# Kernel optimization log

Measured on AMD Instinct MI355X. Metric: run time of the kernel, lower is better.

The kernel has to match this reference:

```python
import jax, jax.numpy as jnp
import numpy as np

N = 8192   # number of points
K = 16     # knn_graph k (loop=True -> self included)
C = 256    # conv hidden width
H = 128    # classifier hidden width


def _lin_init(key, fan_in, fan_out):
    s = 1.0 / np.sqrt(fan_in)
    kw, kb = jax.random.split(key)
    W = jax.random.uniform(kw, (fan_in, fan_out), minval=-s, maxval=s, dtype=jnp.float32)
    b = jax.random.uniform(kb, (fan_out,), minval=-s, maxval=s, dtype=jnp.float32)
    return W, b


def setup_inputs() -> dict:
    key = jax.random.key(0)
    ks = jax.random.split(key, 10)
    pos = jax.random.normal(ks[0], (N, 3), dtype=jnp.float32)
    # conv1 local_nn: Linear(3+3,256), ReLU, Linear(256,256)
    c1_W1, c1_b1 = _lin_init(ks[1], 3 + 3, C)
    c1_W2, c1_b2 = _lin_init(ks[2], C, C)
    # conv2/conv3 local_nn: Linear(256+3,256), ReLU, Linear(256,256)
    c2_W1, c2_b1 = _lin_init(ks[3], C + 3, C)
    c2_W2, c2_b2 = _lin_init(ks[4], C, C)
    c3_W1, c3_b1 = _lin_init(ks[5], C + 3, C)
    c3_W2, c3_b2 = _lin_init(ks[6], C, C)
    # classifier: Linear(256,128), ReLU, Linear(128,128), ReLU, Linear(128,1)
    h_W1, h_b1 = _lin_init(ks[7], C, H)
    h_W2, h_b2 = _lin_init(ks[8], H, H)
    h_W3, h_b3 = _lin_init(ks[9], H, 1)
    return dict(pos=pos,
                c1_W1=c1_W1, c1_b1=c1_b1, c1_W2=c1_W2, c1_b2=c1_b2,
                c2_W1=c2_W1, c2_b1=c2_b1, c2_W2=c2_W2, c2_b2=c2_b2,
                c3_W1=c3_W1, c3_b1=c3_b1, c3_W2=c3_W2, c3_b2=c3_b2,
                h_W1=h_W1, h_b1=h_b1, h_W2=h_W2, h_b2=h_b2, h_W3=h_W3, h_b3=h_b3)


def _knn_idx(pos):
    # squared pairwise distances via the gram trick; [N,N]
    sq = jnp.sum(pos * pos, axis=-1)
    d2 = sq[:, None] + sq[None, :] - 2.0 * (pos @ pos.T)
    # k smallest distances (self distance ~0 -> self loop, matching loop=True)
    _, idx = jax.lax.top_k(-d2, K)  # [N,K] neighbor (source) indices per target
    return idx


def _pointnet_conv(h, rel, idx, W1, b1, W2, b2):
    # message = local_nn(concat(x_j, pos_j - pos_i)); aggregate = max over neighbors
    e = jnp.concatenate([h[idx], rel], axis=-1)          # [N,K,Cin+3]
    m = jax.nn.relu(e @ W1 + b1) @ W2 + b2               # [N,K,C]
    return jnp.max(m, axis=1)                            # [N,C]


def reference(pos,
              c1_W1, c1_b1, c1_W2, c1_b2,
              c2_W1, c2_b1, c2_W2, c2_b2,
              c3_W1, c3_b1, c3_W2, c3_b2,
              h_W1, h_b1, h_W2, h_b2, h_W3, h_b3):
    idx = _knn_idx(pos)
    rel = pos[idx] - pos[:, None, :]                     # [N,K,3] relative coords
    h = pos                                              # train_with_norm=False
    h = jax.nn.relu(_pointnet_conv(h, rel, idx, c1_W1, c1_b1, c1_W2, c1_b2))
    h = jax.nn.relu(_pointnet_conv(h, rel, idx, c2_W1, c2_b1, c2_W2, c2_b2))
    h = jax.nn.relu(_pointnet_conv(h, rel, idx, c3_W1, c3_b1, c3_W2, c3_b2))
    h = jax.nn.relu(h @ h_W1 + h_b1)
    h = jax.nn.relu(h @ h_W2 + h_b2)
    return jax.nn.sigmoid(h @ h_W3 + h_b3)               # [N,1]
```

## Files before the change

### kernel.cpp

```cpp
#include <hip/hip_runtime.h>
#include <hip/hip_bf16.h>
#include <math.h>

#define NPTS 8192
#define CDIM 256
#define HDIM 128
#define NCH  32
#define CH   (NPTS / NCH)
#define CAP  48

typedef __attribute__((ext_vector_type(8))) short bf16x8;
typedef __attribute__((ext_vector_type(4))) float f32x4;
typedef unsigned long long u64;

static __device__ __forceinline__ short f2bf(float f) {
  __hip_bfloat16 h = __float2bfloat16(f);
  return *reinterpret_cast<short*>(&h);
}
static __device__ __forceinline__ float bf2f(short s) {
  return __uint_as_float(((unsigned)(unsigned short)s) << 16);
}

static __device__ __forceinline__ unsigned umed3(unsigned a, unsigned b,
                                                 unsigned c) {
  unsigned d;
  asm("v_med3_u32 %0, %1, %2, %3" : "=v"(d) : "v"(a), "v"(b), "v"(c));
  return d;
}

static __device__ __forceinline__ unsigned d2key(float4 p, float4 c) {
  float dot = fmaf(p.x, c.x, fmaf(p.y, c.y, p.z * c.z));
  float d2 = fmaf(-2.0f, dot, p.w + c.w);
  return __float_as_uint(fmaxf(d2, 0.0f));
}

#define U32INIT unsigned b0=~0u,b1=~0u,b2=~0u,b3=~0u,b4=~0u,b5=~0u,b6=~0u, \
                         b7=~0u,b8=~0u,b9=~0u,b10=~0u,b11=~0u,b12=~0u, \
                         b13=~0u,b14=~0u,b15=~0u;
#define U32CHAIN(key) { \
  b15 = umed3(b14, key, b15); b14 = umed3(b13, key, b14); \
  b13 = umed3(b12, key, b13); b12 = umed3(b11, key, b12); \
  b11 = umed3(b10, key, b11); b10 = umed3(b9,  key, b10); \
  b9  = umed3(b8,  key, b9);  b8  = umed3(b7,  key, b8);  \
  b7  = umed3(b6,  key, b7);  b6  = umed3(b5,  key, b6);  \
  b5  = umed3(b4,  key, b5);  b4  = umed3(b3,  key, b4);  \
  b3  = umed3(b2,  key, b3);  b2  = umed3(b1,  key, b2);  \
  b1  = umed3(b0,  key, b1);  b0  = min(b0, key); }

#define KSTEP(s) { bool sw_ = key < k##s; u64 t_ = k##s; \
                   k##s = sw_ ? key : t_; key = sw_ ? t_ : key; }
#define KCHAIN KSTEP(0) KSTEP(1) KSTEP(2) KSTEP(3) KSTEP(4) KSTEP(5) \
               KSTEP(6) KSTEP(7) KSTEP(8) KSTEP(9) KSTEP(10) KSTEP(11) \
               KSTEP(12) KSTEP(13) KSTEP(14) KSTEP(15)
#define KINIT u64 k0=~0ULL,k1=~0ULL,k2=~0ULL,k3=~0ULL,k4=~0ULL,k5=~0ULL, \
                  k6=~0ULL,k7=~0ULL,k8=~0ULL,k9=~0ULL,k10=~0ULL,k11=~0ULL, \
                  k12=~0ULL,k13=~0ULL,k14=~0ULL,k15=~0ULL;

__global__ __launch_bounds__(256) void prep_all(
    const float* __restrict__ c1W2, const float* __restrict__ c2W2,
    const float* __restrict__ c3W2, const float* __restrict__ c2W1,
    const float* __restrict__ c3W1, const float* __restrict__ hW1,
    const float* __restrict__ hW2,
    short* __restrict__ w2f1, short* __restrict__ w2f2,
    short* __restrict__ w2f3, short* __restrict__ wc2a,
    short* __restrict__ wc3a, short* __restrict__ whW1,
    short* __restrict__ whW2,
    const float* __restrict__ pos, float4* __restrict__ pos4,
    const float* __restrict__ c1W1, const float* __restrict__ c1b1,
    short* __restrict__ TU) {
  int b = blockIdx.x, tid = threadIdx.x;
  if (b < 1280) {
    const float* W; short* wf; int rb;
    if (b < 256)       { W = c1W2; wf = w2f1; rb = b; }
    else if (b < 512)  { W = c2W2; wf = w2f2; rb = b - 256; }
    else if (b < 768)  { W = c3W2; wf = w2f3; rb = b - 512; }
    else if (b < 1024) { W = c2W1; wf = wc2a; rb = b - 768; }
    else               { W = c3W1; wf = wc3a; rb = b - 1024; }
    int t = rb * 256 + tid;
    int q = t & 7, l = (t >> 3) & 63, F = t >> 9;
    int ks = F & 7, c16 = F >> 3;
    int k = ks * 32 + ((l >> 4) << 3) + q;
    int c = c16 * 16 + (l & 15);
    wf[t] = f2bf(W[k * 256 + c]);
  } else if (b < 1408) {
    int t = (b - 1280) * 256 + tid;
    int q = t & 7, l = (t >> 3) & 63, F = t >> 9;
    int ks = F & 7, c16 = F >> 3;
    int k = ks * 32 + ((l >> 4) << 3) + q;
    int c = c16 * 16 + (l & 15);
    whW1[t] = f2bf(hW1[k * 128 + c]);
  } else if (b < 1472) {
    int t = (b - 1408) * 256 + tid;
    int q = t & 7, l = (t >> 3) & 63, F = t >> 9;
    int ks = F & 3, c16 = F >> 2;
    int k = ks * 32 + ((l >> 4) << 3) + q;
    int c = c16 * 16 + (l & 15);
    whW2[t] = f2bf(hW2[k * 128 + c]);
  } else if (b < 1504) {
    int i = (b - 1472) * 256 + tid;
    float x = pos[3 * i], y = pos[3 * i + 1], z = pos[3 * i + 2];
    pos4[i] = make_float4(x, y, z, x * x + y * y + z * z);
  } else {
    int c = tid;
    float w0 = c1W1[c]       + c1W1[768 + c];
    float w1 = c1W1[256 + c] + c1W1[1024 + c];
    float w2 = c1W1[512 + c] + c1W1[1280 + c];
    float bv = c1b1[c];
    int i0 = (b - 1504) * 16;
#pragma unroll
    for (int r = 0; r < 16; ++r) {
      int i = i0 + r;
      float x = pos[3 * i], y = pos[3 * i + 1], z = pos[3 * i + 2];
      TU[(size_t)i * 256 + c] = f2bf(fmaf(x, w0, fmaf(y, w1, fmaf(z, w2, bv))));
    }
  }
}

__global__ __launch_bounds__(256) void knn_d2p1(const float4* __restrict__ pos4,
                                                unsigned* __restrict__ v) {
  int ch = blockIdx.x & (NCH - 1);
  int i  = (blockIdx.x >> 5) * 256 + threadIdx.x;
  const float4* cb = pos4 + ch * CH;

  float4 p = pos4[i];
  U32INIT
  for (int jj = 0; jj < CH; jj += 4) {
    float4 c0 = cb[jj], c1 = cb[jj + 1], c2 = cb[jj + 2], c3 = cb[jj + 3];
    unsigned x0 = d2key(p, c0), x1 = d2key(p, c1);
    unsigned x2 = d2key(p, c2), x3 = d2key(p, c3);
    U32CHAIN(x0) U32CHAIN(x1) U32CHAIN(x2) U32CHAIN(x3)
  }
  uint4* dst = reinterpret_cast<uint4*>(v + ((size_t)ch * NPTS + i) * 16);
  dst[0] = make_uint4(b0, b1, b2, b3);
  dst[1] = make_uint4(b4, b5, b6, b7);
  dst[2] = make_uint4(b8, b9, b10, b11);
  dst[3] = make_uint4(b12, b13, b14, b15);
}

__global__ __launch_bounds__(256) void knn_merge(const unsigned* __restrict__ v,
                                                 unsigned* __restrict__ T,
                                                 unsigned* __restrict__ cnt) {
  int wv = threadIdx.x >> 6, lane = threadIdx.x & 63;
  int i = blockIdx.x * 4 + wv;
  int ch = lane >> 1, half = lane & 1;
  const uint4* src = reinterpret_cast<const uint4*>(
      v + ((size_t)ch * NPTS + i) * 16 + half * 8);
  uint4 a = src[0], b = src[1];
  unsigned r1 = a.y, r2 = a.z, r3 = a.w;
  unsigned r4 = b.x, r5 = b.y, r6 = b.z, r7 = b.w;
  unsigned h = a.x;
  unsigned wmin = 0;
#pragma unroll
  for (int round = 0; round < 16; ++round) {
    unsigned m = h;
    m = min(m, (unsigned)__shfl_xor((int)m, 1));
    m = min(m, (unsigned)__shfl_xor((int)m, 2));
    m = min(m, (unsigned)__shfl_xor((int)m, 4));
    m = min(m, (unsigned)__shfl_xor((int)m, 8));
    m = min(m, (unsigned)__shfl_xor((int)m, 16));
    m = min(m, (unsigned)__shfl_xor((int)m, 32));
    wmin = m;
    u64 ball = __ballot(h == m);
    bool adv = (lane == __ffsll(ball) - 1);
    h  = adv ? r1 : h;
    r1 = adv ? r2 : r1;
    r2 = adv ? r3 : r2;
    r3 = adv ? r4 : r3;
    r4 = adv ? r5 : r4;
    r5 = adv ? r6 : r5;
    r6 = adv ? r7 : r6;
    r7 = adv ? 0xFFFFFFFFu : r7;
  }
  if (lane == 0) { T[i] = wmin; cnt[i] = 0; }
}

__global__ __launch_bounds__(256) void knn_d2p2(const float4* __restrict__ pos4,
                                                const unsigned* __restrict__ T,
                                                unsigned* __restrict__ cnt,
                                                u64* __restrict__ cbuf) {
  int ch = blockIdx.x & (NCH - 1);
  int i  = (blockIdx.x >> 5) * 256 + threadIdx.x;
  const float4* cb = pos4 + ch * CH;

  float4 p = pos4[i];
  unsigned Ti = T[i];
  int jb = ch * CH;
  for (int jj = 0; jj < CH; jj += 8) {
    unsigned k[8];
#pragma unroll
    for (int u = 0; u < 8; ++u) k[u] = d2key(p, cb[jj + u]);
    unsigned m = min(min(min(k[0], k[1]), min(k[2], k[3])),
                     min(min(k[4], k[5]), min(k[6], k[7])));
    if (m <= Ti) {
#pragma unroll
      for (int u = 0; u < 8; ++u) {
        if (k[u] <= Ti) {
          unsigned slot = atomicAdd(&cnt[i], 1u);
          if (slot < CAP)
            cbuf[(size_t)i * CAP + slot] =
                ((u64)k[u] << 32) | (unsigned)(jb + jj + u);
        }
      }
    }
  }
}

__global__ __launch_bounds__(256) void knn_select(const unsigned* __restrict__ cnt,
                                                  const u64* __restrict__ cbuf,
                                                  int* __restrict__ idx_out) {
  int i = blockIdx.x * 256 + threadIdx.x;
  int c = (int)min(cnt[i], (unsigned)CAP);
  KINIT
#pragma unroll 1
  for (int q = 0; q < c; ++q) {
    u64 key = cbuf[(size_t)i * CAP + q];
    if (key < k15) { KCHAIN }
  }
  int* o = idx_out + i * 16;
  o[0]=(int)(unsigned)k0;   o[1]=(int)(unsigned)k1;   o[2]=(int)(unsigned)k2;
  o[3]=(int)(unsigned)k3;   o[4]=(int)(unsigned)k4;   o[5]=(int)(unsigned)k5;
  o[6]=(int)(unsigned)k6;   o[7]=(int)(unsigned)k7;   o[8]=(int)(unsigned)k8;
  o[9]=(int)(unsigned)k9;   o[10]=(int)(unsigned)k10; o[11]=(int)(unsigned)k11;
  o[12]=(int)(unsigned)k12; o[13]=(int)(unsigned)k13; o[14]=(int)(unsigned)k14;
  o[15]=(int)(unsigned)k15;
}

template <int NCOLS, int KDIM, int ACT, int ADDP, int OUTBF>
__global__ __launch_bounds__(256) void gemm_mfma(
    const short* __restrict__ A,
    const short* __restrict__ wf,
    const float* __restrict__ bias,
    const float* __restrict__ pos,
    const float* __restrict__ W1p,
    void* __restrict__ outp) {
  constexpr int KS = KDIM / 32;
  constexpr int NF = NCOLS / 64;
  __shared__ __align__(16) short As[32 * KDIM];

  int tid = threadIdx.x;
  int row0 = blockIdx.x * 32;

  {
    int row = tid & 31, wq = tid >> 5;
    const short* Ar = A + (size_t)(row0 + row) * KDIM;
#pragma unroll
    for (int q = 0; q < KDIM / 64; ++q) {
      int c0 = wq * 8 + q * 64;
      bf16x8 o = *reinterpret_cast<const bf16x8*>(Ar + c0);
      int byte = row * (KDIM * 2) + c0 * 2;
      byte ^= (row & 7) << 4;
      *reinterpret_cast<bf16x8*>(reinterpret_cast<char*>(As) + byte) = o;
    }
  }
  __syncthreads();

  int l = tid & 63, w = tid >> 6;
  int lhi = l >> 4, llo = l & 15;
  f32x4 zero = {0.f, 0.f, 0.f, 0.f};
  f32x4 acc[2][NF];
#pragma unroll
  for (int m = 0; m < 2; ++m)
#pragma unroll
    for (int n = 0; n < NF; ++n) acc[m][n] = zero;

  const bf16x8* WfV = reinterpret_cast<const bf16x8*>(wf);
#pragma unroll
  for (int ks = 0; ks < KS; ++ks) {
    bf16x8 af[2], bfr[NF];
#pragma unroll
    for (int m = 0; m < 2; ++m) {
      int r = m * 16 + llo;
      int byte = r * (KDIM * 2) + ks * 64 + lhi * 16;
      byte ^= (r & 7) << 4;
      af[m] = *reinterpret_cast<const bf16x8*>(
          reinterpret_cast<const char*>(As) + byte);
    }
#pragma unroll
    for (int n = 0; n < NF; ++n)
      bfr[n] = WfV[((w * NF + n) * KS + ks) * 64 + l];
#pragma unroll
    for (int m = 0; m < 2; ++m)
#pragma unroll
      for (int n = 0; n < NF; ++n)
        acc[m][n] = __builtin_amdgcn_mfma_f32_16x16x32_bf16(af[m], bfr[n],
                                                            acc[m][n], 0, 0, 0);
  }

  int cc[NF];
  float bv[NF], u0[NF], u1[NF], u2[NF];
#pragma unroll
  for (int n = 0; n < NF; ++n) {
    cc[n] = (w * NF + n) * 16 + llo;
    bv[n] = bias[cc[n]];
    if constexpr (ADDP) {
      u0[n] = W1p[cc[n]];
      u1[n] = W1p[NCOLS + cc[n]];
      u2[n] = W1p[2 * NCOLS + cc[n]];
    } else { u0[n] = u1[n] = u2[n] = 0.f; }
  }
#pragma unroll
  for (int m = 0; m < 2; ++m)
#pragma unroll
    for (int j = 0; j < 4; ++j) {
      int r = row0 + m * 16 + lhi * 4 + j;
      float px = 0.f, py = 0.f, pz = 0.f;
      if constexpr (ADDP) { px = pos[3*r]; py = pos[3*r+1]; pz = pos[3*r+2]; }
#pragma unroll
      for (int n = 0; n < NF; ++n) {
        float v = acc[m][n][j] + bv[n];
        if constexpr (ADDP) v += px * u0[n] + py * u1[n] + pz * u2[n];
        if (ACT == 1) v = fmaxf(v, 0.0f);
        if constexpr (OUTBF)
          ((short*)outp)[(size_t)r * NCOLS + cc[n]] = f2bf(v);
        else
          ((float*)outp)[(size_t)r * NCOLS + cc[n]] = v;
      }
    }
}

__global__ __launch_bounds__(256) void conv_mfma(
    const short* __restrict__ TU,
    const float* __restrict__ pos,
    const int* __restrict__ idx,
    const float* __restrict__ W1p,
    const short* __restrict__ w2f,
    const float* __restrict__ b2,
    short* __restrict__ hout) {
  __shared__ __align__(16) short m1s[64 * 256];
  __shared__ float Ub[4][256];
  __shared__ int js[64];

  int tid = threadIdx.x;
  int t0 = blockIdx.x * 4;
  if (tid < 64) js[tid] = idx[(t0 + (tid >> 4)) * 16 + (tid & 15)];
#pragma unroll
  for (int q = 0; q < 4; ++q) {
    int e = tid + 256 * q;
    int tg = e >> 8, c = e & 255;
    float x = pos[3 * (t0 + tg)], y = pos[3 * (t0 + tg) + 1],
          z = pos[3 * (t0 + tg) + 2];
    Ub[tg][c] = x * W1p[c] + y * W1p[256 + c] + z * W1p[512 + c];
  }
  __syncthreads();

  {
    int row = tid & 63;
    int wq = tid >> 6;
    int jrow = js[row];
    const short* TUj = TU + (size_t)jrow * 256;
    const float* Ui = &Ub[row >> 4][0];
#pragma unroll
    for (int q = 0; q < 8; ++q) {
      int c0 = wq * 8 + q * 32;
      bf16x8 tv = *reinterpret_cast<const bf16x8*>(TUj + c0);
      float4 ua = *reinterpret_cast<const float4*>(Ui + c0);
      float4 ub = *reinterpret_cast<const float4*>(Ui + c0 + 4);
      bf16x8 o;
      o[0] = f2bf(fmaxf(bf2f(tv[0]) - ua.x, 0.f));
      o[1] = f2bf(fmaxf(bf2f(tv[1]) - ua.y, 0.f));
      o[2] = f2bf(fmaxf(bf2f(tv[2]) - ua.z, 0.f));
      o[3] = f2bf(fmaxf(bf2f(tv[3]) - ua.w, 0.f));
      o[4] = f2bf(fmaxf(bf2f(tv[4]) - ub.x, 0.f));
      o[5] = f2bf(fmaxf(bf2f(tv[5]) - ub.y, 0.f));
      o[6] = f2bf(fmaxf(bf2f(tv[6]) - ub.z, 0.f));
      o[7] = f2bf(fmaxf(bf2f(tv[7]) - ub.w, 0.f));
      int byte = row * 512 + c0 * 2;
      byte ^= (row & 7) << 4;
      *reinterpret_cast<bf16x8*>(reinterpret_cast<char*>(m1s) + byte) = o;
    }
  }
  __syncthreads();

  int l = tid & 63, w = tid >> 6;
  int lhi = l >> 4, llo = l & 15;
  f32x4 zero = {0.f, 0.f, 0.f, 0.f};
  f32x4 acc[4][4];
#pragma unroll
  for (int m = 0; m < 4; ++m)
#pragma unroll
    for (int n = 0; n < 4; ++n) acc[m][n] = zero;

  const bf16x8* Wf = reinterpret_cast<const bf16x8*>(w2f);
#pragma unroll
  for (int ks = 0; ks < 8; ++ks) {
    int k0 = ks * 32;
    bf16x8 af[4], bfr[4];
#pragma unroll
    for (int m = 0; m < 4; ++m) {
      int r = m * 16 + llo;
      int byte = r * 512 + k0 * 2 + lhi * 16;
      byte ^= (r & 7) << 4;
      af[m] = *reinterpret_cast<const bf16x8*>(
          reinterpret_cast<const char*>(m1s) + byte);
    }
#pragma unroll
    for (int n = 0; n < 4; ++n)
      bfr[n] = Wf[((w * 4 + n) * 8 + ks) * 64 + l];
#pragma unroll
    for (int m = 0; m < 4; ++m)
#pragma unroll
      for (int n = 0; n < 4; ++n)
        acc[m][n] = __builtin_amdgcn_mfma_f32_16x16x32_bf16(af[m], bfr[n],
                                                            acc[m][n], 0, 0, 0);
  }

#pragma unroll
  for (int m = 0; m < 4; ++m)
#pragma unroll
    for (int n = 0; n < 4; ++n) {
      float v = fmaxf(fmaxf(acc[m][n][0], acc[m][n][1]),
                      fmaxf(acc[m][n][2], acc[m][n][3]));
      v = fmaxf(v, __shfl_xor(v, 16));
      v = fmaxf(v, __shfl_xor(v, 32));
      if (lhi == 0) {
        int c = w * 64 + n * 16 + llo;
        hout[(size_t)(t0 + m) * CDIM + c] = f2bf(fmaxf(v + b2[c], 0.0f));
      }
    }
}

__global__ __launch_bounds__(64) void final_k(const float* __restrict__ h2,
                                              const float* __restrict__ w3,
                                              const float* __restrict__ b3,
                                              float* __restrict__ out) {
  int r = blockIdx.x, l = threadIdx.x;
  float s = h2[(size_t)r * HDIM + l] * w3[l] +
            h2[(size_t)r * HDIM + 64 + l] * w3[64 + l];
#pragma unroll
  for (int o = 32; o > 0; o >>= 1) s += __shfl_down(s, o);
  if (l == 0) out[r] = 1.0f / (1.0f + expf(-(s + b3[0])));
}

extern "C" void kernel_launch(void* const* d_in, const int* in_sizes, int n_in,
                              void* d_out, int out_size, void* d_ws,
                              size_t ws_size, hipStream_t stream) {
  const float* pos   = (const float*)d_in[0];
  const float* c1_W1 = (const float*)d_in[1];
  const float* c1_b1 = (const float*)d_in[2];
  const float* c1_W2 = (const float*)d_in[3];
  const float* c1_b2 = (const float*)d_in[4];
  const float* c2_W1 = (const float*)d_in[5];
  const float* c2_b1 = (const float*)d_in[6];
  const float* c2_W2 = (const float*)d_in[7];
  const float* c2_b2 = (const float*)d_in[8];
  const float* c3_W1 = (const float*)d_in[9];
  const float* c3_b1 = (const float*)d_in[10];
  const float* c3_W2 = (const float*)d_in[11];
  const float* c3_b2 = (const float*)d_in[12];
  const float* h_W1  = (const float*)d_in[13];
  const float* h_b1  = (const float*)d_in[14];
  const float* h_W2  = (const float*)d_in[15];
  const float* h_b2  = (const float*)d_in[16];
  const float* h_W3  = (const float*)d_in[17];
  const float* h_b3  = (const float*)d_in[18];
  float* out = (float*)d_out;

  char* w = (char*)d_ws;
  const size_t MB = 1 << 20;
  const size_t KB = 1 << 10;
  int*      p_idx  = (int*)w;
  float4*   p_pos4 = (float4*)(w + 512 * KB);
  unsigned* p_T    = (unsigned*)(w + 640 * KB);
  unsigned* p_cnt  = (unsigned*)(w + 672 * KB);
  short*    p_w2f1 = (short*)(w + 704 * KB);
  short*    p_w2f2 = (short*)(w + 832 * KB);
  short*    p_w2f3 = (short*)(w + 960 * KB);
  short*    p_wc2a = (short*)(w + 1088 * KB);
  short*    p_wc3a = (short*)(w + 1216 * KB);
  short*    p_whW1 = (short*)(w + 1344 * KB);
  short*    p_whW2 = (short*)(w + 1408 * KB);
  u64*      p_cbuf = (u64*)(w + 1536 * KB);
  short*    p_TU   = (short*)(w + 5 * MB);
  short*    p_c1   = (short*)(w + 9 * MB);
  unsigned* p_v    = (unsigned*)(w + 13 * MB);
  short*    p_hA   = (short*)(w + 13 * MB);
  short*    p_hB   = (short*)(w + 21 * MB);
  float*    p_c2   = (float*)(w + 29 * MB);

  prep_all<<<2016, 256, 0, stream>>>(
      c1_W2, c2_W2, c3_W2, c2_W1, c3_W1, h_W1, h_W2,
      p_w2f1, p_w2f2, p_w2f3, p_wc2a, p_wc3a, p_whW1, p_whW2,
      pos, p_pos4, c1_W1, c1_b1, p_TU);

  knn_d2p1<<<(NPTS / 256) * NCH, 256, 0, stream>>>(p_pos4, p_v);
  knn_merge<<<NPTS / 4, 256, 0, stream>>>(p_v, p_T, p_cnt);
  knn_d2p2<<<(NPTS / 256) * NCH, 256, 0, stream>>>(p_pos4, p_T, p_cnt, p_cbuf);
  knn_select<<<NPTS / 256, 256, 0, stream>>>(p_cnt, p_cbuf, p_idx);

  conv_mfma<<<NPTS / 4, 256, 0, stream>>>(p_TU, pos, p_idx, c1_W1 + 3 * 256,
                                          p_w2f1, c1_b2, p_hA);
  gemm_mfma<256, 256, 0, 1, 1><<<NPTS / 32, 256, 0, stream>>>(
      p_hA, p_wc2a, c2_b1, pos, c2_W1 + 256 * 256, p_TU);
  conv_mfma<<<NPTS / 4, 256, 0, stream>>>(p_TU, pos, p_idx, c2_W1 + 256 * 256,
                                          p_w2f2, c2_b2, p_hB);
  gemm_mfma<256, 256, 0, 1, 1><<<NPTS / 32, 256, 0, stream>>>(
      p_hB, p_wc3a, c3_b1, pos, c3_W1 + 256 * 256, p_TU);
  conv_mfma<<<NPTS / 4, 256, 0, stream>>>(p_TU, pos, p_idx, c3_W1 + 256 * 256,
                                          p_w2f3, c3_b2, p_hA);
  gemm_mfma<128, 256, 1, 0, 1><<<NPTS / 32, 256, 0, stream>>>(
      p_hA, p_whW1, h_b1, nullptr, nullptr, p_c1);
  gemm_mfma<128, 128, 1, 0, 0><<<NPTS / 32, 256, 0, stream>>>(
      p_c1, p_whW2, h_b2, nullptr, nullptr, p_c2);
  final_k<<<NPTS, 64, 0, stream>>>(p_c2, h_W3, h_b3, out);

  (void)in_sizes; (void)n_in; (void)out_size; (void)ws_size;
}
```

Baseline: 252.5 us.

## Build worklist of candidate chunks to skip non-contributing kNN rescans

```diff
diff --git a/kernel.cpp b/kernel.cpp
--- a/kernel.cpp
+++ b/kernel.cpp
@@ -117,7 +117,9 @@
 }
 
 __global__ __launch_bounds__(256) void knn_d2p1(const float4* __restrict__ pos4,
-                                                unsigned* __restrict__ v) {
+                                                unsigned* __restrict__ v,
+                                                unsigned* __restrict__ wcount) {
+  if (blockIdx.x == 0 && threadIdx.x == 0) *wcount = 0u;
   int ch = blockIdx.x & (NCH - 1);
   int i  = (blockIdx.x >> 5) * 256 + threadIdx.x;
   const float4* cb = pos4 + ch * CH;
@@ -139,13 +141,16 @@
 
 __global__ __launch_bounds__(256) void knn_merge(const unsigned* __restrict__ v,
                                                  unsigned* __restrict__ T,
-                                                 unsigned* __restrict__ cnt) {
+                                                 unsigned* __restrict__ cnt,
+                                                 unsigned* __restrict__ wl,
+                                                 unsigned* __restrict__ wcount) {
   int wv = threadIdx.x >> 6, lane = threadIdx.x & 63;
   int i = blockIdx.x * 4 + wv;
   int ch = lane >> 1, half = lane & 1;
   const uint4* src = reinterpret_cast<const uint4*>(
       v + ((size_t)ch * NPTS + i) * 16 + half * 8);
   uint4 a = src[0], b = src[1];
+  unsigned first = a.x;
   unsigned r1 = a.y, r2 = a.z, r3 = a.w;
   unsigned r4 = b.x, r5 = b.y, r6 = b.z, r7 = b.w;
   unsigned h = a.x;
@@ -172,33 +177,51 @@
     r7 = adv ? 0xFFFFFFFFu : r7;
   }
   if (lane == 0) { T[i] = wmin; cnt[i] = 0; }
+
+  u64 fb = __ballot(first <= wmin);
+  u64 pairb = fb | (fb >> 1);
+  bool emit = (half == 0) && ((pairb >> lane) & 1ull);
+  u64 eb = __ballot(emit);
+  unsigned nadd = (unsigned)__popcll(eb);
+  unsigned base = 0;
+  if (lane == 0 && nadd) base = atomicAdd(wcount, nadd);
+  base = (unsigned)__shfl((int)base, 0);
+  if (emit) {
+    int rank = __popcll(eb & ((lane == 63) ? ~0ull >> 1 : ((1ull << lane) - 1)));
+    wl[base + rank] = ((unsigned)i << 5) | (unsigned)ch;
+  }
 }
 
 __global__ __launch_bounds__(256) void knn_d2p2(const float4* __restrict__ pos4,
                                                 const unsigned* __restrict__ T,
                                                 unsigned* __restrict__ cnt,
+                                                const unsigned* __restrict__ wl,
+                                                const unsigned* __restrict__ wcount,
                                                 u64* __restrict__ cbuf) {
-  int ch = blockIdx.x & (NCH - 1);
-  int i  = (blockIdx.x >> 5) * 256 + threadIdx.x;
-  const float4* cb = pos4 + ch * CH;
-
-  float4 p = pos4[i];
-  unsigned Ti = T[i];
-  int jb = ch * CH;
-  for (int jj = 0; jj < CH; jj += 8) {
-    unsigned k[8];
-#pragma unroll
-    for (int u = 0; u < 8; ++u) k[u] = d2key(p, cb[jj + u]);
-    unsigned m = min(min(min(k[0], k[1]), min(k[2], k[3])),
-                     min(min(k[4], k[5]), min(k[6], k[7])));
-    if (m <= Ti) {
-#pragma unroll
-      for (int u = 0; u < 8; ++u) {
-        if (k[u] <= Ti) {
-          unsigned slot = atomicAdd(&cnt[i], 1u);
-          if (slot < CAP)
-            cbuf[(size_t)i * CAP + slot] =
-                ((u64)k[u] << 32) | (unsigned)(jb + jj + u);
+  int n = (int)*wcount;
+  for (int e = blockIdx.x * 256 + threadIdx.x; e < n; e += 1024 * 256) {
+    unsigned ent = wl[e];
+    int i = (int)(ent >> 5);
+    int ch = (int)(ent & 31u);
+    float4 p = pos4[i];
+    unsigned Ti = T[i];
+    const float4* cb = pos4 + ch * CH;
+    int jb = ch * CH;
+    for (int jj = 0; jj < CH; jj += 8) {
+      unsigned k[8];
+#pragma unroll
+      for (int u = 0; u < 8; ++u) k[u] = d2key(p, cb[jj + u]);
+      unsigned m = min(min(min(k[0], k[1]), min(k[2], k[3])),
+                       min(min(k[4], k[5]), min(k[6], k[7])));
+      if (m <= Ti) {
+#pragma unroll
+        for (int u = 0; u < 8; ++u) {
+          if (k[u] <= Ti) {
+            unsigned slot = atomicAdd(&cnt[i], 1u);
+            if (slot < CAP)
+              cbuf[(size_t)i * CAP + slot] =
+                  ((u64)k[u] << 32) | (unsigned)(jb + jj + u);
+          }
         }
       }
     }
@@ -469,9 +492,11 @@
   short*    p_wc3a = (short*)(w + 1216 * KB);
   short*    p_whW1 = (short*)(w + 1344 * KB);
   short*    p_whW2 = (short*)(w + 1408 * KB);
-  u64*      p_cbuf = (u64*)(w + 1536 * KB);
-  short*    p_TU   = (short*)(w + 5 * MB);
-  short*    p_c1   = (short*)(w + 9 * MB);
+  unsigned* p_wcnt = (unsigned*)(w + 1440 * KB);
+  unsigned* p_wl   = (unsigned*)(w + 1536 * KB);
+  u64*      p_cbuf = (u64*)(w + 2560 * KB);
+  short*    p_TU   = (short*)(w + 6 * MB);
+  short*    p_c1   = (short*)(w + 10 * MB);
   unsigned* p_v    = (unsigned*)(w + 13 * MB);
   short*    p_hA   = (short*)(w + 13 * MB);
   short*    p_hB   = (short*)(w + 21 * MB);
@@ -482,9 +507,9 @@
       p_w2f1, p_w2f2, p_w2f3, p_wc2a, p_wc3a, p_whW1, p_whW2,
       pos, p_pos4, c1_W1, c1_b1, p_TU);
 
-  knn_d2p1<<<(NPTS / 256) * NCH, 256, 0, stream>>>(p_pos4, p_v);
-  knn_merge<<<NPTS / 4, 256, 0, stream>>>(p_v, p_T, p_cnt);
-  knn_d2p2<<<(NPTS / 256) * NCH, 256, 0, stream>>>(p_pos4, p_T, p_cnt, p_cbuf);
+  knn_d2p1<<<(NPTS / 256) * NCH, 256, 0, stream>>>(p_pos4, p_v, p_wcnt);
+  knn_merge<<<NPTS / 4, 256, 0, stream>>>(p_v, p_T, p_cnt, p_wl, p_wcnt);
+  knn_d2p2<<<1024, 256, 0, stream>>>(p_pos4, p_T, p_cnt, p_wl, p_wcnt, p_cbuf);
   knn_select<<<NPTS / 256, 256, 0, stream>>>(p_cnt, p_cbuf, p_idx);
 
   conv_mfma<<<NPTS / 4, 256, 0, stream>>>(p_TU, pos, p_idx, c1_W1 + 3 * 256,
```

Result: slower. 371.2 us (+47.0%).
